# Performance work log

Measured on AMD Instinct MI355X. Metric: run time of the kernel, lower is better.

The kernel has to match this reference:

```python
import jax, jax.numpy as jnp
import numpy as np

B, N, D, OUT, NUM_ITERS = 8, 4096, 1024, 1024, 3
LN_EPS = 1e-5


def setup_inputs() -> dict:
    key = jax.random.key(0)
    ks = jax.random.split(key, 8)
    s = (6.0 / (2 * D)) ** 0.5  # xavier-uniform-like scale
    return {
        "query": jax.random.normal(ks[0], (B, D), jnp.float32),
        "feat": jax.random.normal(ks[1], (B, N, D), jnp.float32),
        "W_h": jax.random.uniform(ks[2], (D, D), jnp.float32, -s, s),
        "W_f": jax.random.uniform(ks[3], (D, D), jnp.float32, -s, s),
        "W_g": jax.random.normal(ks[4], (4, D, D), jnp.float32) / np.sqrt(D),
        "ln_w": jnp.ones((D,), jnp.float32),
        "ln_b": jnp.zeros((D,), jnp.float32),
        "W_out": jax.random.uniform(ks[5], (OUT, D), jnp.float32, -s, s),
        "b_out": jnp.zeros((OUT,), jnp.float32),
        "feat_mask": jax.random.bernoulli(ks[6], 0.2, (B, 1, 1, N)),
    }


def _layer_norm(x, w, b):
    mu = x.mean(-1, keepdims=True)
    var = jnp.var(x, axis=-1, keepdims=True)
    return (x - mu) / jnp.sqrt(var + LN_EPS) * w + b


def reference(query, feat, W_h, W_f, W_g, ln_w, ln_b, W_out, b_out, feat_mask):
    q = query @ W_h                       # [B, D]
    f = feat @ W_f                        # [B, N, D]
    mask = feat_mask.reshape(feat.shape[0], feat.shape[1])  # squeeze(1).squeeze(1)
    b = jnp.where(mask, jnp.float32(-1e18), jnp.float32(0.0))  # [B, N]
    # feat_group is iteration-invariant: mean over the 4 orthogonal transforms
    # mean_g(f @ W_g[g].T) == f @ mean_g(W_g).T
    fg = f @ W_g.mean(0).T                # [B, N, D]
    n = fg.shape[1]
    for i in range(NUM_ITERS):
        c = jax.nn.softmax(b, axis=1)     # [B, N]
        if i == NUM_ITERS - 1:
            out = jnp.einsum('bn,bnd->bd', c, fg)
        else:
            delta = jnp.einsum('bd,bnd->bn', q, fg)
            delta = (delta - delta.mean(1, keepdims=True)) / (
                delta.std(1, keepdims=True, ddof=1) + 1e-9)  # torch.std is unbiased
            b = b + delta
            out = jnp.einsum('bn,bnd->bd', c, fg) / n  # mean over dim 1
        q = _layer_norm(q + jax.nn.selu(out), ln_w, ln_b)
    return q @ W_out.T + b_out
```

## Files before the change

### kernel.cpp

```cpp
#include <hip/hip_runtime.h>
#include <hip/hip_bf16.h>


using u16 = unsigned short;
using u32 = unsigned int;
using u8  = unsigned char;
using u64 = unsigned long long;

#define SELU_L 1.0507009873554805f
#define SELU_A 1.6732632423543772f

__device__ float g_M[1048576];
__device__ float g_q[8192];
__device__ float g_tus[24576];
__device__ float g_bst[32768];
__device__ float g_c[32768];
__device__ float g_delta[32768];
__device__ float g_outv[8192];
__device__ float g_v[8192];
__device__ int   g_dt[12];

__device__ __forceinline__ float blo(u32 u){ return __uint_as_float(u << 16); }
__device__ __forceinline__ float bhi(u32 u){ return __uint_as_float(u & 0xffff0000u); }
__device__ __forceinline__ float b2f(u16 u){ return __uint_as_float(((u32)u) << 16); }

__device__ __forceinline__ void unpack8(uint4 x, float* f){
  f[0]=blo(x.x); f[1]=bhi(x.x); f[2]=blo(x.y); f[3]=bhi(x.y);
  f[4]=blo(x.z); f[5]=bhi(x.z); f[6]=blo(x.w); f[7]=bhi(x.w);
}

__device__ __forceinline__ float ldf(const void* p, size_t i, int dt){
  return dt ? ((const float*)p)[i] : b2f(((const u16*)p)[i]);
}
__device__ __forceinline__ void load8(const void* base, size_t idx, int dt, float* f){
  if (dt == 0) {
    uint4 x = *(const uint4*)((const u16*)base + idx);
    unpack8(x, f);
  } else {
    const float* p = (const float*)base + idx;
    float4 a = *(const float4*)p, b = *(const float4*)(p + 4);
    f[0]=a.x; f[1]=a.y; f[2]=a.z; f[3]=a.w; f[4]=b.x; f[5]=b.y; f[6]=b.z; f[7]=b.w;
  }
}

__device__ __forceinline__ float wredsum(float x){
#pragma unroll
  for (int o = 32; o; o >>= 1) x += __shfl_xor(x, o, 64);
  return x;
}

__global__ void kdet(const void* p0, const void* p1, const void* p2, const void* p3,
                     const void* p4, const void* p5, const void* p6, const void* p7,
                     const void* p8, const void* p9)
{
  const void* ps[10] = {p0,p1,p2,p3,p4,p5,p6,p7,p8,p9};
  int tid = threadIdx.x;
  int w = tid >> 6, lane = tid & 63;
  if (w < 9) {
    const u16* wp = (const u16*)ps[w];
    u16 x0 = wp[lane], x1 = wp[64 + lane];
    int e0 = (x0 >> 7) & 0xFF, e1 = (x1 >> 7) & 0xFF;
    u64 nz0 = __ballot(x0 != 0), nz1 = __ballot(x1 != 0);
    u64 pa0 = __ballot(x0 != 0 && e0 >= 0x70 && e0 <= 0x8F);
    u64 pa1 = __ballot(x1 != 0 && e1 >= 0x70 && e1 <= 0x8F);
    if (lane == 0) {
      const u64 evenm = 0x5555555555555555ULL;
      int nz = __popcll(nz0) + __popcll(nz1);
      int pass = __popcll(pa0) + __popcll(pa1);
      int evenNZ = __popcll(nz0 & evenm) + __popcll(nz1 & evenm);
      int oddNZ  = nz - evenNZ;
      int dt;
      if (nz == 0)                    dt = 0;
      else if (evenNZ == 0 && oddNZ)  dt = 1;
      else                            dt = (pass * 10 >= nz * 9) ? 0 : 1;
      g_dt[w] = dt;
    }
  } else if (w == 9) {
    const u8* mp = (const u8*)ps[9];
    u64 v = ((const u64*)mp)[lane];
    bool f16c=false, isF=false, nz01=false, nzNon4=false, nzM8_4=false, anynz=false;
#pragma unroll
    for (int j = 0; j < 8; ++j) {
      u8 cb = (u8)(v >> (8 * j));
      if (!cb) continue;
      int i = lane * 8 + j;
      anynz = true;
      if (cb == 0x3C && (i & 1)) f16c = true;
      if (cb == 0x3F || cb == 0x80) isF = true;
      int m = i & 3;
      if (m == 0 || m == 1) nz01 = true;
      if (m != 0) nzNon4 = true;
      if ((i & 7) == 4) nzM8_4 = true;
    }
    bool A  = __ballot(f16c)   != 0;
    bool Bf = __ballot(isF)    != 0;
    bool C  = __ballot(nz01)   != 0;
    bool Dn = __ballot(nzNon4) != 0;
    bool E  = __ballot(nzM8_4) != 0;
    bool F  = __ballot(anynz)  != 0;
    if (lane == 0) {
      int mode;
      if (A)       mode = 4;
      else if (Bf) mode = C ? 2 : 3;
      else if (Dn) mode = 0;
      else if (E)  mode = 1;
      else if (F)  mode = 5;
      else         mode = 1;
      g_dt[9] = mode;
    }
  }
  for (int i = tid; i < 8192; i += 640) g_q[i] = 0.f;
}

__global__ void kzero() {
  int i = (blockIdx.x * 256 + threadIdx.x) * 4;
  *(float4*)(g_tus + i) = make_float4(0.f, 0.f, 0.f, 0.f);
}

__global__ void kprep(const void* __restrict__ Wg, const void* __restrict__ Wh,
                      const void* __restrict__ query, const u8* __restrict__ maskp)
{
  int blk = blockIdx.x, tid = threadIdx.x;
  if (blk < 1024) {
    int dtg = g_dt[4];
    int e = blk * 1024 + tid * 4;
    float a0=0.f,a1=0.f,a2=0.f,a3=0.f;
#pragma unroll
    for (int g = 0; g < 4; ++g) {
      size_t o = (size_t)g * 1048576 + e;
      a0 += ldf(Wg, o+0, dtg); a1 += ldf(Wg, o+1, dtg);
      a2 += ldf(Wg, o+2, dtg); a3 += ldf(Wg, o+3, dtg);
    }
    *(float4*)(g_M + e) = make_float4(a0*0.25f, a1*0.25f, a2*0.25f, a3*0.25f);
  } else if (blk < 1088) {
    int dtq = g_dt[0], dth = g_dt[2];
    __shared__ float ql[512];
    int blk2 = blk - 1024;
    int kt = blk2 & 3, dc = blk2 >> 2;
    for (int idx = tid; idx < 512; idx += 256) {
      int b = idx >> 6, d = idx & 63;
      ql[idx] = ldf(query, b * 1024 + dc * 64 + d, dtq);
    }
    __syncthreads();
    int k = kt * 256 + tid;
    float acc[8] = {0,0,0,0,0,0,0,0};
    for (int dd = 0; dd < 64; ++dd) {
      int d = dc * 64 + dd;
      float w = ldf(Wh, (size_t)d * 1024 + k, dth);
#pragma unroll
      for (int b = 0; b < 8; ++b) acc[b] += ql[(b << 6) + dd] * w;
    }
#pragma unroll
    for (int b = 0; b < 8; ++b) atomicAdd(&g_q[b * 1024 + k], acc[b]);
  } else {
    int mode = g_dt[9];
    int e0 = (blk - 1088) * 1024 + tid * 4;
#pragma unroll
    for (int j = 0; j < 4; ++j) {
      int e = e0 + j;
      bool on;
      if (mode == 0)      on = maskp[e] != 0;
      else if (mode == 1) on = ((const int*)maskp)[e] != 0;
      else if (mode == 2) on = ((const u16*)maskp)[e] != 0;
      else if (mode == 3) on = ((const u32*)maskp)[e] != 0;
      else if (mode == 4) on = ((const u16*)maskp)[e] != 0;
      else                on = ((const u64*)maskp)[e] != 0ULL;
      g_bst[e] = on ? -1e18f : 0.f;
    }
  }
}

__global__ void ksm(int do_t)
{
  __shared__ float sm[1024];
  int blk = blockIdx.x, tid = threadIdx.x;
  float* t = g_tus;
  if (blk < 8) {
    int b = blk;
    const float* row = g_bst + b * 4096;
    float mx = -3.4e38f;
    for (int i = tid; i < 4096; i += 256) mx = fmaxf(mx, row[i]);
    sm[tid] = mx; __syncthreads();
    for (int s2 = 128; s2; s2 >>= 1) { if (tid < s2) sm[tid] = fmaxf(sm[tid], sm[tid + s2]); __syncthreads(); }
    mx = sm[0]; __syncthreads();
    float sum = 0.f;
    for (int i = tid; i < 4096; i += 256) {
      float e = __expf(row[i] - mx);
      g_c[b * 4096 + i] = e; sum += e;
    }
    sm[tid] = sum; __syncthreads();
    for (int s2 = 128; s2; s2 >>= 1) { if (tid < s2) sm[tid] += sm[tid + s2]; __syncthreads(); }
    float inv = 1.f / sm[0];
    for (int i = tid; i < 4096; i += 256) g_c[b * 4096 + i] *= inv;
  } else {
    int blk2 = blk - 8;
    int jt = blk2 & 3, dc = blk2 >> 2;
    for (int idx = tid; idx < 512; idx += 256) {
      int b = idx >> 6, d = idx & 63;
      sm[idx] = g_q[b * 1024 + dc * 64 + d];
    }
    __syncthreads();
    int j = jt * 256 + tid;
    float acc[8] = {0,0,0,0,0,0,0,0};
    for (int dd = 0; dd < 64; ++dd) {
      int d = dc * 64 + dd;
      float mv = g_M[(size_t)d * 1024 + j];
#pragma unroll
      for (int b = 0; b < 8; ++b) acc[b] += sm[(b << 6) + dd] * mv;
    }
#pragma unroll
    for (int b = 0; b < 8; ++b) atomicAdd(&t[b * 1024 + j], acc[b]);
  }
}

__global__ void kv(const void* __restrict__ Wf)
{
  __shared__ float tl[8192];
  int tid = threadIdx.x;
  int dtf = g_dt[3];
  for (int i = tid; i < 8192; i += 256) tl[i] = g_tus[i];
  __syncthreads();
  int w = tid >> 6, lane = tid & 63;
  int k = blockIdx.x * 4 + w;
  size_t row = (size_t)k * 1024;
  float f[16];
  load8(Wf, row + lane * 8, dtf, f);
  load8(Wf, row + 512 + lane * 8, dtf, f + 8);
  float acc[8];
#pragma unroll
  for (int b = 0; b < 8; ++b) {
    const float* tb = tl + b * 1024;
    float d = 0.f;
#pragma unroll
    for (int j = 0; j < 8; ++j) d += f[j]     * tb[lane * 8 + j];
#pragma unroll
    for (int j = 0; j < 8; ++j) d += f[8 + j] * tb[512 + lane * 8 + j];
    acc[b] = wredsum(d);
  }
  if (lane == 0) {
#pragma unroll
    for (int b = 0; b < 8; ++b) g_v[b * 1024 + k] = acc[b];
  }
}

__global__ void __launch_bounds__(256)
kfeat(const void* __restrict__ feat, int need_delta)
{
  __shared__ float sl[4][1024];
  int tid = threadIdx.x, w = tid >> 6, lane = tid & 63;
  int b = blockIdx.x >> 6, ch = blockIdx.x & 63;
  int dtf = g_dt[1];
  float* s = g_tus + 16384;
  float vr[16];
#pragma unroll
  for (int j = 0; j < 16; ++j) vr[j] = 0.f;
  if (need_delta) {
    const float* vb = g_v + b * 1024;
#pragma unroll
    for (int j = 0; j < 8; ++j) { vr[j] = vb[lane * 8 + j]; vr[8 + j] = vb[512 + lane * 8 + j]; }
  }
  float acc[16];
#pragma unroll
  for (int j = 0; j < 16; ++j) acc[j] = 0.f;
  int n0 = ch * 64 + w * 16;
  for (int r = 0; r < 16; ++r) {
    int n = n0 + r;
    size_t row = ((size_t)b * 4096 + n) * 1024;
    float f[16];
    load8(feat, row + lane * 8, dtf, f);
    load8(feat, row + 512 + lane * 8, dtf, f + 8);
    float cn = g_c[b * 4096 + n];
#pragma unroll
    for (int j = 0; j < 16; ++j) acc[j] += cn * f[j];
    if (need_delta) {
      float dot = 0.f;
#pragma unroll
      for (int j = 0; j < 16; ++j) dot += f[j] * vr[j];
      dot = wredsum(dot);
      if (lane == 0) g_delta[b * 4096 + n] = dot;
    }
  }
#pragma unroll
  for (int j = 0; j < 8; ++j) {
    sl[w][lane * 8 + j] = acc[j];
    sl[w][512 + lane * 8 + j] = acc[8 + j];
  }
  __syncthreads();
#pragma unroll
  for (int j = 0; j < 4; ++j) {
    int k = tid * 4 + j;
    float val = sl[0][k] + sl[1][k] + sl[2][k] + sl[3][k];
    atomicAdd(&s[b * 1024 + k], val);
  }
}

__global__ void kpost(const void* __restrict__ Wf, int do_stats)
{
  __shared__ float sm[1024];
  int blk = blockIdx.x, tid = threadIdx.x;
  float* u = g_tus + 8192;
  float* s = g_tus + 16384;
  if (do_stats && blk < 8) {
    int b = blk;
    const float* row = g_delta + b * 4096;
    float xs[16], sum = 0.f, sq = 0.f;
#pragma unroll
    for (int r = 0; r < 16; ++r) { float x = row[tid + 256 * r]; xs[r] = x; sum += x; sq += x * x; }
    sm[tid] = sum; __syncthreads();
    for (int s2 = 128; s2; s2 >>= 1) { if (tid < s2) sm[tid] += sm[tid + s2]; __syncthreads(); }
    sum = sm[0]; __syncthreads();
    sm[tid] = sq; __syncthreads();
    for (int s2 = 128; s2; s2 >>= 1) { if (tid < s2) sm[tid] += sm[tid + s2]; __syncthreads(); }
    sq = sm[0];
    float mean = sum / 4096.f;
    float var = fmaxf((sq - 4096.f * mean * mean) / 4095.f, 0.f);
    float inv = 1.f / (sqrtf(var) + 1e-9f);
#pragma unroll
    for (int r = 0; r < 16; ++r) {
      int i = tid + 256 * r;
      g_bst[b * 4096 + i] += (xs[r] - mean) * inv;
    }
  } else {
    int dtf = g_dt[3];
    int blk2 = blk - (do_stats ? 8 : 0);
    int jt = blk2 & 3, kc = blk2 >> 2;
    for (int idx = tid; idx < 512; idx += 256) {
      int b = idx >> 6, kk = idx & 63;
      sm[idx] = s[b * 1024 + kc * 64 + kk];
    }
    __syncthreads();
    int j = jt * 256 + tid;
    float acc[8] = {0,0,0,0,0,0,0,0};
    for (int kk = 0; kk < 64; ++kk) {
      int k = kc * 64 + kk;
      float w = ldf(Wf, (size_t)k * 1024 + j, dtf);
#pragma unroll
      for (int b = 0; b < 8; ++b) acc[b] += sm[(b << 6) + kk] * w;
    }
#pragma unroll
    for (int b = 0; b < 8; ++b) atomicAdd(&u[b * 1024 + j], acc[b]);
  }
}

__global__ void kout()
{
  __shared__ float ul[8192];
  int tid = threadIdx.x;
  for (int i = tid; i < 8192; i += 256) ul[i] = g_tus[8192 + i];
  __syncthreads();
  int w = tid >> 6, lane = tid & 63;
  int d = blockIdx.x * 4 + w;
  const float* row = g_M + (size_t)d * 1024;
  float f[16];
#pragma unroll
  for (int cc = 0; cc < 4; ++cc) {
    float4 x = *(const float4*)(row + cc * 256 + lane * 4);
    f[cc*4+0]=x.x; f[cc*4+1]=x.y; f[cc*4+2]=x.z; f[cc*4+3]=x.w;
  }
  float acc[8];
#pragma unroll
  for (int b = 0; b < 8; ++b) {
    const float* ub = ul + b * 1024;
    float dd = 0.f;
#pragma unroll
    for (int cc = 0; cc < 4; ++cc)
#pragma unroll
      for (int e = 0; e < 4; ++e) dd += f[cc * 4 + e] * ub[cc * 256 + lane * 4 + e];
    acc[b] = wredsum(dd);
  }
  if (lane == 0) {
#pragma unroll
    for (int b = 0; b < 8; ++b) g_outv[b * 1024 + d] = acc[b];
  }
}

__global__ void kq(const void* __restrict__ lnw, const void* __restrict__ lnb,
                   float scale)
{
  __shared__ float sm[256];
  int b = blockIdx.x, tid = threadIdx.x;
  int dtw = g_dt[5], dtb = g_dt[6];
  float x[4], sum = 0.f, sq = 0.f;
#pragma unroll
  for (int j = 0; j < 4; ++j) {
    int d = tid * 4 + j;
    float o = g_outv[b * 1024 + d] * scale;
    float se = (o > 0.f) ? SELU_L * o : SELU_L * SELU_A * expm1f(o);
    float val = g_q[b * 1024 + d] + se;
    x[j] = val; sum += val; sq += val * val;
  }
  sm[tid] = sum; __syncthreads();
  for (int s2 = 128; s2; s2 >>= 1) { if (tid < s2) sm[tid] += sm[tid + s2]; __syncthreads(); }
  sum = sm[0]; __syncthreads();
  sm[tid] = sq; __syncthreads();
  for (int s2 = 128; s2; s2 >>= 1) { if (tid < s2) sm[tid] += sm[tid + s2]; __syncthreads(); }
  sq = sm[0];
  float mean = sum / 1024.f;
  float var = fmaxf(sq / 1024.f - mean * mean, 0.f);
  float rstd = rsqrtf(var + 1e-5f);
#pragma unroll
  for (int j = 0; j < 4; ++j) {
    int d = tid * 4 + j;
    g_q[b * 1024 + d] = (x[j] - mean) * rstd * ldf(lnw, d, dtw) + ldf(lnb, d, dtb);
  }
}

__global__ void kfin(const void* __restrict__ Wout, const void* __restrict__ bout,
                     float* __restrict__ out)
{
  __shared__ float ql[8192];
  int tid = threadIdx.x;
  int dto = g_dt[7], dtb = g_dt[8];
  for (int i = tid; i < 8192; i += 256) ql[i] = g_q[i];
  __syncthreads();
  int w = tid >> 6, lane = tid & 63;
  int o = blockIdx.x * 4 + w;
  size_t row = (size_t)o * 1024;
  float f[16];
  load8(Wout, row + lane * 8, dto, f);
  load8(Wout, row + 512 + lane * 8, dto, f + 8);
  float acc[8];
#pragma unroll
  for (int b = 0; b < 8; ++b) {
    const float* qb = ql + b * 1024;
    float d = 0.f;
#pragma unroll
    for (int j = 0; j < 8; ++j) d += f[j]     * qb[lane * 8 + j];
#pragma unroll
    for (int j = 0; j < 8; ++j) d += f[8 + j] * qb[512 + lane * 8 + j];
    acc[b] = wredsum(d);
  }
  if (lane == 0) {
    float bo = ldf(bout, o, dtb);
#pragma unroll
    for (int b = 0; b < 8; ++b) out[b * 1024 + o] = acc[b] + bo;
  }
}

extern "C" void kernel_launch(void* const* d_in, const int* in_sizes, int n_in,
                              void* d_out, int out_size, void* d_ws, size_t ws_size,
                              hipStream_t stream)
{
  const void* query = d_in[0];
  const void* feat  = d_in[1];
  const void* Wh    = d_in[2];
  const void* Wf    = d_in[3];
  const void* Wg    = d_in[4];
  const void* lnw   = d_in[5];
  const void* lnb   = d_in[6];
  const void* Wout  = d_in[7];
  const void* bout  = d_in[8];
  const u8*   maskp = (const u8*)d_in[9];
  (void)in_sizes; (void)n_in; (void)out_size; (void)d_ws; (void)ws_size;

  kdet<<<1, 640, 0, stream>>>(query, feat, Wh, Wf, Wg, lnw, lnb, Wout, bout, maskp);
  kprep<<<1120, 256, 0, stream>>>(Wg, Wh, query, maskp);

  for (int i = 0; i < 3; ++i) {
    int nl = (i < 2);
    kzero<<<24, 256, 0, stream>>>();
    ksm<<<8 + (nl ? 64 : 0), 256, 0, stream>>>(nl);
    if (nl) kv<<<256, 256, 0, stream>>>(Wf);
    kfeat<<<512, 256, 0, stream>>>(feat, nl);
    kpost<<<(nl ? 8 : 0) + 64, 256, 0, stream>>>(Wf, nl);
    kout<<<256, 256, 0, stream>>>();
    kq<<<8, 256, 0, stream>>>(lnw, lnb, nl ? (1.f / 4096.f) : 1.f);
  }
  kfin<<<256, 256, 0, stream>>>(Wout, bout, (float*)d_out);
}
```

Baseline: 431.7 us.

## Fuse all stages into a single cooperative persistent kernel with grid syncs

Replaces the sequence of roughly twenty small kernel launches with one cooperative kernel of 256 blocks that walks all stages, separating them with grid-wide synchronisation. Zeroing of accumulators is folded into otherwise idle blocks of earlier phases. This removes per-launch overhead and inter-kernel gaps, at the cost of a fixed, smaller grid (fewer waves in flight for the large feat streaming pass) and the latency of each grid barrier. The old multi-kernel path is kept as a fallback if the cooperative launch fails.

```diff
diff --git a/kernel.cpp b/kernel.cpp
--- a/kernel.cpp
+++ b/kernel.cpp
@@ -1,6 +1,8 @@
 #include <hip/hip_runtime.h>
-#include <hip/hip_bf16.h>
-
+#include <hip/hip_cooperative_groups.h>
+
+
+namespace cg = cooperative_groups;
 
 using u16 = unsigned short;
 using u32 = unsigned int;
@@ -10,14 +12,14 @@
 #define SELU_L 1.0507009873554805f
 #define SELU_A 1.6732632423543772f
 
-__device__ float g_M[1048576];
-__device__ float g_q[8192];
-__device__ float g_tus[24576];
-__device__ float g_bst[32768];
-__device__ float g_c[32768];
-__device__ float g_delta[32768];
-__device__ float g_outv[8192];
-__device__ float g_v[8192];
+__device__ __align__(16) float g_M[1048576];
+__device__ __align__(16) float g_q[8192];
+__device__ __align__(16) float g_tus[24576];
+__device__ __align__(16) float g_bst[32768];
+__device__ __align__(16) float g_c[32768];
+__device__ __align__(16) float g_delta[32768];
+__device__ __align__(16) float g_outv[8192];
+__device__ __align__(16) float g_v[8192];
 __device__ int   g_dt[12];
 
 __device__ __forceinline__ float blo(u32 u){ return __uint_as_float(u << 16); }
@@ -28,7 +30,6 @@
   f[0]=blo(x.x); f[1]=bhi(x.x); f[2]=blo(x.y); f[3]=bhi(x.y);
   f[4]=blo(x.z); f[5]=bhi(x.z); f[6]=blo(x.w); f[7]=bhi(x.w);
 }
-
 __device__ __forceinline__ float ldf(const void* p, size_t i, int dt){
   return dt ? ((const float*)p)[i] : b2f(((const u16*)p)[i]);
 }
@@ -42,20 +43,13 @@
     f[0]=a.x; f[1]=a.y; f[2]=a.z; f[3]=a.w; f[4]=b.x; f[5]=b.y; f[6]=b.z; f[7]=b.w;
   }
 }
-
 __device__ __forceinline__ float wredsum(float x){
 #pragma unroll
   for (int o = 32; o; o >>= 1) x += __shfl_xor(x, o, 64);
   return x;
 }
 
-__global__ void kdet(const void* p0, const void* p1, const void* p2, const void* p3,
-                     const void* p4, const void* p5, const void* p6, const void* p7,
-                     const void* p8, const void* p9)
-{
-  const void* ps[10] = {p0,p1,p2,p3,p4,p5,p6,p7,p8,p9};
-  int tid = threadIdx.x;
-  int w = tid >> 6, lane = tid & 63;
+__device__ __forceinline__ void sniff_wave(const void* const* ps, int w, int lane){
   if (w < 9) {
     const u16* wp = (const u16*)ps[w];
     u16 x0 = wp[lane], x1 = wp[64 + lane];
@@ -109,6 +103,349 @@
       g_dt[9] = mode;
     }
   }
+}
+
+__device__ __forceinline__ bool mask_on(const u8* maskp, int e, int mode){
+  if (mode == 0)      return maskp[e] != 0;
+  else if (mode == 1) return ((const int*)maskp)[e] != 0;
+  else if (mode == 2) return ((const u16*)maskp)[e] != 0;
+  else if (mode == 3) return ((const u32*)maskp)[e] != 0;
+  else if (mode == 4) return ((const u16*)maskp)[e] != 0;
+  else                return ((const u64*)maskp)[e] != 0ULL;
+}
+
+__global__ void __launch_bounds__(256, 2)
+kfused(const void* query, const void* feat, const void* Wh, const void* Wf,
+       const void* Wg, const void* lnw, const void* lnb, const void* Wout,
+       const void* bout, const u8* maskp, float* out)
+{
+  cg::grid_group grid = cg::this_grid();
+  __shared__ float sm[8192];
+  const int blk = blockIdx.x, tid = threadIdx.x;
+  const int wv = tid >> 6, lane = tid & 63;
+  const void* ps[10] = {query, feat, Wh, Wf, Wg, lnw, lnb, Wout, bout, (const void*)maskp};
+
+  if (blk < 3) {
+    sniff_wave(ps, blk * 4 + wv, lane);
+  } else if (blk >= 4 && blk < 36) {
+    int i = (blk - 4) * 1024 + tid * 4;
+    float4 z = make_float4(0.f, 0.f, 0.f, 0.f);
+    if (i < 8192) *(float4*)(g_q + i) = z;
+    else          *(float4*)(g_tus + (i - 8192)) = z;
+  }
+  __threadfence(); grid.sync();
+
+  {
+    const int dtg = g_dt[4];
+#pragma unroll
+    for (int rep = 0; rep < 2; ++rep) {
+      int e = blk * 4096 + rep * 2048 + tid * 8;
+      float acc[8] = {0,0,0,0,0,0,0,0};
+#pragma unroll
+      for (int g = 0; g < 4; ++g) {
+        float f[8];
+        load8(Wg, (size_t)g * 1048576 + e, dtg, f);
+#pragma unroll
+        for (int j = 0; j < 8; ++j) acc[j] += f[j];
+      }
+      *(float4*)(g_M + e)     = make_float4(acc[0]*0.25f, acc[1]*0.25f, acc[2]*0.25f, acc[3]*0.25f);
+      *(float4*)(g_M + e + 4) = make_float4(acc[4]*0.25f, acc[5]*0.25f, acc[6]*0.25f, acc[7]*0.25f);
+    }
+  }
+  if (blk < 64) {
+    const int dtq = g_dt[0], dth = g_dt[2];
+    int kt = blk & 3, dc = blk >> 2;
+    for (int idx = tid; idx < 512; idx += 256) {
+      int b = idx >> 6, d = idx & 63;
+      sm[idx] = ldf(query, b * 1024 + dc * 64 + d, dtq);
+    }
+    __syncthreads();
+    int k = kt * 256 + tid;
+    float acc[8] = {0,0,0,0,0,0,0,0};
+    for (int dd = 0; dd < 64; ++dd) {
+      int d = dc * 64 + dd;
+      float w = ldf(Wh, (size_t)d * 1024 + k, dth);
+#pragma unroll
+      for (int b = 0; b < 8; ++b) acc[b] += sm[(b << 6) + dd] * w;
+    }
+#pragma unroll
+    for (int b = 0; b < 8; ++b) atomicAdd(&g_q[b * 1024 + k], acc[b]);
+  } else if (blk < 96) {
+    int mode = g_dt[9];
+    int e0 = (blk - 64) * 1024 + tid * 4;
+#pragma unroll
+    for (int j = 0; j < 4; ++j) {
+      int e = e0 + j;
+      g_bst[e] = mask_on(maskp, e, mode) ? -1e18f : 0.f;
+    }
+  }
+  __threadfence(); grid.sync();
+
+  float* t = g_tus;
+  float* u = g_tus + 8192;
+  float* s = g_tus + 16384;
+
+  for (int it = 0; it < 3; ++it) {
+    const int nl = (it < 2);
+
+    if (blk < 8) {
+      int b = blk;
+      const float* row = g_bst + b * 4096;
+      float mx = -3.4e38f;
+      for (int i = tid; i < 4096; i += 256) mx = fmaxf(mx, row[i]);
+      sm[tid] = mx; __syncthreads();
+      for (int s2 = 128; s2; s2 >>= 1) { if (tid < s2) sm[tid] = fmaxf(sm[tid], sm[tid + s2]); __syncthreads(); }
+      mx = sm[0]; __syncthreads();
+      float sum = 0.f;
+      for (int i = tid; i < 4096; i += 256) {
+        float e = __expf(row[i] - mx);
+        g_c[b * 4096 + i] = e; sum += e;
+      }
+      sm[tid] = sum; __syncthreads();
+      for (int s2 = 128; s2; s2 >>= 1) { if (tid < s2) sm[tid] += sm[tid + s2]; __syncthreads(); }
+      float inv = 1.f / sm[0];
+      for (int i = tid; i < 4096; i += 256) g_c[b * 4096 + i] *= inv;
+    } else if (nl && blk < 72) {
+      int blk2 = blk - 8;
+      int jt = blk2 & 3, dc = blk2 >> 2;
+      for (int idx = tid; idx < 512; idx += 256) {
+        int b = idx >> 6, d = idx & 63;
+        sm[idx] = g_q[b * 1024 + dc * 64 + d];
+      }
+      __syncthreads();
+      int j = jt * 256 + tid;
+      float acc[8] = {0,0,0,0,0,0,0,0};
+      for (int dd = 0; dd < 64; ++dd) {
+        int d = dc * 64 + dd;
+        float mv = g_M[(size_t)d * 1024 + j];
+#pragma unroll
+        for (int b = 0; b < 8; ++b) acc[b] += sm[(b << 6) + dd] * mv;
+      }
+#pragma unroll
+      for (int b = 0; b < 8; ++b) atomicAdd(&t[b * 1024 + j], acc[b]);
+    }
+    __threadfence(); grid.sync();
+
+    if (nl) {
+      const int dtf = g_dt[3];
+      for (int i = tid; i < 8192; i += 256) sm[i] = t[i];
+      __syncthreads();
+      int k = blk * 4 + wv;
+      size_t row = (size_t)k * 1024;
+      float f[16];
+      load8(Wf, row + lane * 8, dtf, f);
+      load8(Wf, row + 512 + lane * 8, dtf, f + 8);
+      float acc[8];
+#pragma unroll
+      for (int b = 0; b < 8; ++b) {
+        const float* tb = sm + b * 1024;
+        float d = 0.f;
+#pragma unroll
+        for (int j = 0; j < 8; ++j) d += f[j]     * tb[lane * 8 + j];
+#pragma unroll
+        for (int j = 0; j < 8; ++j) d += f[8 + j] * tb[512 + lane * 8 + j];
+        acc[b] = wredsum(d);
+      }
+      if (lane == 0) {
+#pragma unroll
+        for (int b = 0; b < 8; ++b) g_v[b * 1024 + k] = acc[b];
+      }
+      __threadfence(); grid.sync();
+    }
+
+    {
+      const int dtf = g_dt[1];
+      int b = blk >> 5, ch = blk & 31;
+      float vr[16];
+#pragma unroll
+      for (int j = 0; j < 16; ++j) vr[j] = 0.f;
+      if (nl) {
+        const float* vb = g_v + b * 1024;
+#pragma unroll
+        for (int j = 0; j < 8; ++j) { vr[j] = vb[lane * 8 + j]; vr[8 + j] = vb[512 + lane * 8 + j]; }
+      }
+      float acc[16];
+#pragma unroll
+      for (int j = 0; j < 16; ++j) acc[j] = 0.f;
+      int n0 = ch * 128 + wv * 32;
+      for (int r = 0; r < 32; ++r) {
+        int n = n0 + r;
+        size_t row = ((size_t)b * 4096 + n) * 1024;
+        float f[16];
+        load8(feat, row + lane * 8, dtf, f);
+        load8(feat, row + 512 + lane * 8, dtf, f + 8);
+        float cn = g_c[b * 4096 + n];
+#pragma unroll
+        for (int j = 0; j < 16; ++j) acc[j] += cn * f[j];
+        if (nl) {
+          float dot = 0.f;
+#pragma unroll
+          for (int j = 0; j < 16; ++j) dot += f[j] * vr[j];
+          dot = wredsum(dot);
+          if (lane == 0) g_delta[b * 4096 + n] = dot;
+        }
+      }
+#pragma unroll
+      for (int j = 0; j < 8; ++j) {
+        sm[wv * 1024 + lane * 8 + j]       = acc[j];
+        sm[wv * 1024 + 512 + lane * 8 + j] = acc[8 + j];
+      }
+      __syncthreads();
+#pragma unroll
+      for (int j = 0; j < 4; ++j) {
+        int k = tid * 4 + j;
+        float val = sm[k] + sm[1024 + k] + sm[2048 + k] + sm[3072 + k];
+        atomicAdd(&s[b * 1024 + k], val);
+      }
+    }
+    __threadfence(); grid.sync();
+
+    if (nl && blk < 8) {
+      int b = blk;
+      const float* row = g_delta + b * 4096;
+      float xs[16], sum = 0.f, sq = 0.f;
+#pragma unroll
+      for (int r = 0; r < 16; ++r) { float x = row[tid + 256 * r]; xs[r] = x; sum += x; sq += x * x; }
+      sm[tid] = sum; __syncthreads();
+      for (int s2 = 128; s2; s2 >>= 1) { if (tid < s2) sm[tid] += sm[tid + s2]; __syncthreads(); }
+      sum = sm[0]; __syncthreads();
+      sm[tid] = sq; __syncthreads();
+      for (int s2 = 128; s2; s2 >>= 1) { if (tid < s2) sm[tid] += sm[tid + s2]; __syncthreads(); }
+      sq = sm[0];
+      float mean = sum / 4096.f;
+      float var = fmaxf((sq - 4096.f * mean * mean) / 4095.f, 0.f);
+      float inv = 1.f / (sqrtf(var) + 1e-9f);
+#pragma unroll
+      for (int r = 0; r < 16; ++r) {
+        int i = tid + 256 * r;
+        g_bst[b * 4096 + i] += (xs[r] - mean) * inv;
+      }
+    } else if (blk >= 8 && blk < 72) {
+      const int dtf = g_dt[3];
+      int blk2 = blk - 8;
+      int jt = blk2 & 3, kc = blk2 >> 2;
+      for (int idx = tid; idx < 512; idx += 256) {
+        int b = idx >> 6, kk = idx & 63;
+        sm[idx] = s[b * 1024 + kc * 64 + kk];
+      }
+      __syncthreads();
+      int j = jt * 256 + tid;
+      float acc[8] = {0,0,0,0,0,0,0,0};
+      for (int kk = 0; kk < 64; ++kk) {
+        int k = kc * 64 + kk;
+        float w = ldf(Wf, (size_t)k * 1024 + j, dtf);
+#pragma unroll
+        for (int b = 0; b < 8; ++b) acc[b] += sm[(b << 6) + kk] * w;
+      }
+#pragma unroll
+      for (int b = 0; b < 8; ++b) atomicAdd(&u[b * 1024 + j], acc[b]);
+    } else if (nl && blk >= 72 && blk < 80) {
+      int i = (blk - 72) * 1024 + tid * 4;
+      *(float4*)(t + i) = make_float4(0.f, 0.f, 0.f, 0.f);
+    }
+    __threadfence(); grid.sync();
+
+    {
+      for (int i = tid; i < 8192; i += 256) sm[i] = u[i];
+      __syncthreads();
+      int d = blk * 4 + wv;
+      const float* row = g_M + (size_t)d * 1024;
+      float f[16];
+#pragma unroll
+      for (int cc = 0; cc < 4; ++cc) {
+        float4 x = *(const float4*)(row + cc * 256 + lane * 4);
+        f[cc*4+0]=x.x; f[cc*4+1]=x.y; f[cc*4+2]=x.z; f[cc*4+3]=x.w;
+      }
+      float acc[8];
+#pragma unroll
+      for (int b = 0; b < 8; ++b) {
+        const float* ub = sm + b * 1024;
+        float dd = 0.f;
+#pragma unroll
+        for (int cc = 0; cc < 4; ++cc)
+#pragma unroll
+          for (int e = 0; e < 4; ++e) dd += f[cc * 4 + e] * ub[cc * 256 + lane * 4 + e];
+        acc[b] = wredsum(dd);
+      }
+      if (lane == 0) {
+#pragma unroll
+        for (int b = 0; b < 8; ++b) g_outv[b * 1024 + d] = acc[b];
+      }
+    }
+    __threadfence(); grid.sync();
+
+    if (blk < 8) {
+      const int dtw = g_dt[5], dtb = g_dt[6];
+      const float scale = nl ? (1.f / 4096.f) : 1.f;
+      int b = blk;
+      float x[4], sum = 0.f, sq = 0.f;
+#pragma unroll
+      for (int j = 0; j < 4; ++j) {
+        int d = tid * 4 + j;
+        float o = g_outv[b * 1024 + d] * scale;
+        float se = (o > 0.f) ? SELU_L * o : SELU_L * SELU_A * expm1f(o);
+        float val = g_q[b * 1024 + d] + se;
+        x[j] = val; sum += val; sq += val * val;
+      }
+      sm[tid] = sum; __syncthreads();
+      for (int s2 = 128; s2; s2 >>= 1) { if (tid < s2) sm[tid] += sm[tid + s2]; __syncthreads(); }
+      sum = sm[0]; __syncthreads();
+      sm[tid] = sq; __syncthreads();
+      for (int s2 = 128; s2; s2 >>= 1) { if (tid < s2) sm[tid] += sm[tid + s2]; __syncthreads(); }
+      sq = sm[0];
+      float mean = sum / 1024.f;
+      float var = fmaxf(sq / 1024.f - mean * mean, 0.f);
+      float rstd = rsqrtf(var + 1e-5f);
+#pragma unroll
+      for (int j = 0; j < 4; ++j) {
+        int d = tid * 4 + j;
+        g_q[b * 1024 + d] = (x[j] - mean) * rstd * ldf(lnw, d, dtw) + ldf(lnb, d, dtb);
+      }
+    } else if (nl && blk >= 8 && blk < 16) {
+      int i = (blk - 8) * 1024 + tid * 4;
+      *(float4*)(u + i) = make_float4(0.f, 0.f, 0.f, 0.f);
+    } else if (nl && blk >= 16 && blk < 24) {
+      int i = (blk - 16) * 1024 + tid * 4;
+      *(float4*)(s + i) = make_float4(0.f, 0.f, 0.f, 0.f);
+    }
+    __threadfence(); grid.sync();
+  }
+
+  {
+    const int dto = g_dt[7], dtb = g_dt[8];
+    for (int i = tid; i < 8192; i += 256) sm[i] = g_q[i];
+    __syncthreads();
+    int o = blk * 4 + wv;
+    size_t row = (size_t)o * 1024;
+    float f[16];
+    load8(Wout, row + lane * 8, dto, f);
+    load8(Wout, row + 512 + lane * 8, dto, f + 8);
+    float acc[8];
+#pragma unroll
+    for (int b = 0; b < 8; ++b) {
+      const float* qb = sm + b * 1024;
+      float d = 0.f;
+#pragma unroll
+      for (int j = 0; j < 8; ++j) d += f[j]     * qb[lane * 8 + j];
+#pragma unroll
+      for (int j = 0; j < 8; ++j) d += f[8 + j] * qb[512 + lane * 8 + j];
+      acc[b] = wredsum(d);
+    }
+    if (lane == 0) {
+      float bo = ldf(bout, o, dtb);
+#pragma unroll
+      for (int b = 0; b < 8; ++b) out[b * 1024 + o] = acc[b] + bo;
+    }
+  }
+}
+
+__global__ void kdet(const void* p0, const void* p1, const void* p2, const void* p3,
+                     const void* p4, const void* p5, const void* p6, const void* p7,
+                     const void* p8, const void* p9)
+{
+  const void* ps[10] = {p0,p1,p2,p3,p4,p5,p6,p7,p8,p9};
+  int tid = threadIdx.x;
+  sniff_wave(ps, tid >> 6, tid & 63);
   for (int i = tid; i < 8192; i += 640) g_q[i] = 0.f;
 }
 
@@ -158,14 +495,7 @@
 #pragma unroll
     for (int j = 0; j < 4; ++j) {
       int e = e0 + j;
-      bool on;
-      if (mode == 0)      on = maskp[e] != 0;
-      else if (mode == 1) on = ((const int*)maskp)[e] != 0;
-      else if (mode == 2) on = ((const u16*)maskp)[e] != 0;
-      else if (mode == 3) on = ((const u32*)maskp)[e] != 0;
-      else if (mode == 4) on = ((const u16*)maskp)[e] != 0;
-      else                on = ((const u64*)maskp)[e] != 0ULL;
-      g_bst[e] = on ? -1e18f : 0.f;
+      g_bst[e] = mask_on(maskp, e, mode) ? -1e18f : 0.f;
     }
   }
 }
@@ -451,20 +781,29 @@
   const void* Wout  = d_in[7];
   const void* bout  = d_in[8];
   const u8*   maskp = (const u8*)d_in[9];
+  float*      outp  = (float*)d_out;
   (void)in_sizes; (void)n_in; (void)out_size; (void)d_ws; (void)ws_size;
 
-  kdet<<<1, 640, 0, stream>>>(query, feat, Wh, Wf, Wg, lnw, lnb, Wout, bout, maskp);
-  kprep<<<1120, 256, 0, stream>>>(Wg, Wh, query, maskp);
-
-  for (int i = 0; i < 3; ++i) {
-    int nl = (i < 2);
-    kzero<<<24, 256, 0, stream>>>();
-    ksm<<<8 + (nl ? 64 : 0), 256, 0, stream>>>(nl);
-    if (nl) kv<<<256, 256, 0, stream>>>(Wf);
-    kfeat<<<512, 256, 0, stream>>>(feat, nl);
-    kpost<<<(nl ? 8 : 0) + 64, 256, 0, stream>>>(Wf, nl);
-    kout<<<256, 256, 0, stream>>>();
-    kq<<<8, 256, 0, stream>>>(lnw, lnb, nl ? (1.f / 4096.f) : 1.f);
-  }
-  kfin<<<256, 256, 0, stream>>>(Wout, bout, (float*)d_out);
-}
+  void* args[11] = {
+    (void*)&query, (void*)&feat, (void*)&Wh, (void*)&Wf, (void*)&Wg,
+    (void*)&lnw, (void*)&lnb, (void*)&Wout, (void*)&bout, (void*)&maskp,
+    (void*)&outp
+  };
+  hipError_t rc = hipLaunchCooperativeKernel((const void*)kfused, dim3(256),
+                                             dim3(256), args, 0, stream);
+  if (rc != hipSuccess) {
+    kdet<<<1, 640, 0, stream>>>(query, feat, Wh, Wf, Wg, lnw, lnb, Wout, bout, maskp);
+    kprep<<<1120, 256, 0, stream>>>(Wg, Wh, query, maskp);
+    for (int i = 0; i < 3; ++i) {
+      int nl = (i < 2);
+      kzero<<<24, 256, 0, stream>>>();
+      ksm<<<8 + (nl ? 64 : 0), 256, 0, stream>>>(nl);
+      if (nl) kv<<<256, 256, 0, stream>>>(Wf);
+      kfeat<<<512, 256, 0, stream>>>(feat, nl);
+      kpost<<<(nl ? 8 : 0) + 64, 256, 0, stream>>>(Wf, nl);
+      kout<<<256, 256, 0, stream>>>();
+      kq<<<8, 256, 0, stream>>>(lnw, lnb, nl ? (1.f / 4096.f) : 1.f);
+    }
+    kfin<<<256, 256, 0, stream>>>(Wout, bout, outp);
+  }
+}
```

Measured after the change: 1.385 ms. +220.7%, slower.
